# Performance work log

Hardware: AMD Instinct MI355X
Metric: run time of the kernel (lower is better)

The kernel has to match this reference:

```python
import jax, jax.numpy as jnp
import numpy as np

D = 128
N_NODES = 50000
N_EDGES = 500000


def layer_norm(x, g, b, eps=1e-5):
    m = jnp.mean(x, axis=-1, keepdims=True)
    v = jnp.var(x, axis=-1, keepdims=True)
    return (x - m) * jax.lax.rsqrt(v + eps) * g + b


def setup_inputs() -> dict:
    key = jax.random.key(0)
    ks = jax.random.split(key, 10)
    s = 1.0 / np.sqrt(D)  # torch Linear default-ish init scale
    return {
        "src": jax.random.normal(ks[0], (N_NODES, D), jnp.float32),
        "tgt": jax.random.normal(ks[1], (N_NODES, D), jnp.float32),
        "edge": jax.random.normal(ks[2], (N_EDGES, D), jnp.float32),
        "src_idx": jax.random.randint(ks[3], (N_EDGES,), 0, N_NODES, jnp.int64 if jax.config.jax_enable_x64 else jnp.int32),
        "tgt_idx": jax.random.randint(ks[4], (N_EDGES,), 0, N_NODES, jnp.int64 if jax.config.jax_enable_x64 else jnp.int32),
        "W_s2e": jax.random.normal(ks[5], (D, D), jnp.float32) * s,
        "W_t2e": jax.random.normal(ks[6], (D, D), jnp.float32) * s,
        "W_e2e": jax.random.normal(ks[7], (D, D), jnp.float32) * s,
        "W_e2t": jax.random.normal(ks[8], (D, D), jnp.float32) * s,
        "W_t2t": jax.random.normal(ks[9], (D, D), jnp.float32) * s,
        "ln1_g": jnp.ones((D,), jnp.float32),
        "ln1_b": jnp.zeros((D,), jnp.float32),
        "ln2_g": jnp.ones((D,), jnp.float32),
        "ln2_b": jnp.zeros((D,), jnp.float32),
    }


def reference(src, tgt, edge, src_idx, tgt_idx,
              W_s2e, W_t2e, W_e2e, W_e2t, W_t2t,
              ln1_g, ln1_b, ln2_g, ln2_b):
    # ---- STE2E: source/target/edge -> edge update ----
    # gather endpoint node features per edge [E, D]
    msg = (src[src_idx] @ W_s2e.T
           + tgt[tgt_idx] @ W_t2e.T
           + edge @ W_e2e.T)
    edge_out = edge + layer_norm(jax.nn.silu(msg), ln1_g, ln1_b)

    # ---- ET2T: aggregate edges to target nodes, update targets ----
    agg = jax.ops.segment_sum(edge_out, tgt_idx, num_segments=tgt.shape[0])  # [N, D]
    tgt_msg = agg @ W_e2t.T + tgt @ W_t2t.T
    tgt_out = tgt + layer_norm(jax.nn.silu(tgt_msg), ln2_g, ln2_b)

    return edge_out, tgt_out
```

## Files before the change

### kernel.cpp

```cpp
#include <hip/hip_runtime.h>
#include <hip/hip_bf16.h>

#define D 128
#define LDSPAD 136

typedef short s8v __attribute__((ext_vector_type(8)));
typedef float f4v __attribute__((ext_vector_type(4)));

__device__ inline short f2bf(float f) {
    __hip_bfloat16 h = __float2bfloat16(f);
    return *reinterpret_cast<short*>(&h);
}

__device__ inline void load_w_lds(const float* __restrict__ W, short* lds) {
    const int tid = threadIdx.x;
    const float4* W4 = reinterpret_cast<const float4*>(W);
#pragma unroll
    for (int i = 0; i < 16; ++i) {
        int f = tid + 256 * i;
        float4 v = W4[f];
        int row = f >> 5;
        int c4  = (f & 31) * 4;
        short* p = &lds[row * LDSPAD + c4];
        p[0] = f2bf(v.x); p[1] = f2bf(v.y);
        p[2] = f2bf(v.z); p[3] = f2bf(v.w);
    }
}

__device__ inline void mfma_tile(const float* __restrict__ X, int row0,
                                 const short* lds, f4v acc[8]) {
    const int lane = threadIdx.x & 63;
    const int l15 = lane & 15, q = lane >> 4;
    s8v a[4];
    const float* xr = X + (size_t)(row0 + l15) * D + q * 8;
#pragma unroll
    for (int c = 0; c < 4; ++c) {
        float4 f0 = *reinterpret_cast<const float4*>(xr + c * 32);
        float4 f1 = *reinterpret_cast<const float4*>(xr + c * 32 + 4);
        s8v t;
        t[0] = f2bf(f0.x); t[1] = f2bf(f0.y); t[2] = f2bf(f0.z); t[3] = f2bf(f0.w);
        t[4] = f2bf(f1.x); t[5] = f2bf(f1.y); t[6] = f2bf(f1.z); t[7] = f2bf(f1.w);
        a[c] = t;
    }
#pragma unroll
    for (int t = 0; t < 8; ++t) {
        f4v acc_t = {0.f, 0.f, 0.f, 0.f};
#pragma unroll
        for (int c = 0; c < 4; ++c) {
            const s8v b = *reinterpret_cast<const s8v*>(
                &lds[(t * 16 + l15) * LDSPAD + c * 32 + q * 8]);
            acc_t = __builtin_amdgcn_mfma_f32_16x16x32_bf16(a[c], b, acc_t, 0, 0, 0);
        }
        acc[t] = acc_t;
    }
}


__global__ __launch_bounds__(256) void k_zero_i(int* p, int n) {
    int i = blockIdx.x * 256 + threadIdx.x;
    if (i < n) p[i] = 0;
}

__global__ __launch_bounds__(256) void k_hist(const int* __restrict__ tidx,
                                              int* __restrict__ cnt, int E) {
    int i = blockIdx.x * 256 + threadIdx.x;
    if (i < E) atomicAdd(&cnt[tidx[i]], 1);
}

__global__ __launch_bounds__(1024) void k_scan(const int* __restrict__ cnt,
                                               int* __restrict__ off,
                                               int* __restrict__ cursor, int n) {
    __shared__ int part[1024];
    const int tid = threadIdx.x;
    const int chunk = (n + 1023) / 1024;
    const int lo = tid * chunk;
    const int hi = min(lo + chunk, n);
    int s = 0;
    for (int i = lo; i < hi; ++i) s += cnt[i];
    part[tid] = s;
    __syncthreads();
    for (int d = 1; d < 1024; d <<= 1) {
        int v = (tid >= d) ? part[tid - d] : 0;
        __syncthreads();
        part[tid] += v;
        __syncthreads();
    }
    int run = part[tid] - s;
    for (int i = lo; i < hi; ++i) {
        off[i] = run;
        cursor[i] = run;
        run += cnt[i];
    }
    if (tid == 0) off[n] = part[1023];
}

__global__ __launch_bounds__(256) void k_scatter(const int* __restrict__ tidx,
                                                 int* __restrict__ cursor,
                                                 int* __restrict__ elist, int E) {
    int i = blockIdx.x * 256 + threadIdx.x;
    if (i < E) {
        int p = atomicAdd(&cursor[tidx[i]], 1);
        elist[p] = i;
    }
}


__global__ __launch_bounds__(256) void k_node_gemm(const float* __restrict__ X,
                                                   const float* __restrict__ W,
                                                   float* __restrict__ P, int nrows) {
    __shared__ short lds[D * LDSPAD];
    load_w_lds(W, lds);
    __syncthreads();
    const int lane = threadIdx.x & 63, wave = threadIdx.x >> 6;
    const int l15 = lane & 15, q = lane >> 4;
    const int ntiles = nrows >> 4;
    for (int tile = blockIdx.x * 4 + wave; tile < ntiles; tile += gridDim.x * 4) {
        f4v acc[8];
        mfma_tile(X, tile * 16, lds, acc);
#pragma unroll
        for (int t = 0; t < 8; ++t) {
            int col = t * 16 + l15;
#pragma unroll
            for (int r = 0; r < 4; ++r)
                P[(size_t)(tile * 16 + q * 4 + r) * D + col] = acc[t][r];
        }
    }
}

__global__ __launch_bounds__(256) void k_edge(const float* __restrict__ edge,
                                              const int* __restrict__ sidx,
                                              const int* __restrict__ tidx,
                                              const float* __restrict__ W,
                                              const float* __restrict__ Ps,
                                              const float* __restrict__ Pt,
                                              const float* __restrict__ g1,
                                              const float* __restrict__ b1,
                                              float* __restrict__ eout, int E) {
    __shared__ short lds[D * LDSPAD];
    load_w_lds(W, lds);
    __syncthreads();
    const int lane = threadIdx.x & 63, wave = threadIdx.x >> 6;
    const int l15 = lane & 15, q = lane >> 4;
    const int ntiles = E >> 4;
    for (int tile = blockIdx.x * 4 + wave; tile < ntiles; tile += gridDim.x * 4) {
        const int e0 = tile * 16;
        f4v acc[8];
        mfma_tile(edge, e0, lds, acc);
        int si[4], ti[4];
#pragma unroll
        for (int r = 0; r < 4; ++r) {
            si[r] = sidx[e0 + q * 4 + r];
            ti[r] = tidx[e0 + q * 4 + r];
        }
        float h[8][4];
        float s1[4] = {0.f, 0.f, 0.f, 0.f}, s2[4] = {0.f, 0.f, 0.f, 0.f};
#pragma unroll
        for (int t = 0; t < 8; ++t) {
            int col = t * 16 + l15;
#pragma unroll
            for (int r = 0; r < 4; ++r) {
                float m = acc[t][r] + Ps[(size_t)si[r] * D + col]
                                    + Pt[(size_t)ti[r] * D + col];
                float hh = m / (1.f + __expf(-m));
                h[t][r] = hh;
                s1[r] += hh;
                s2[r] += hh * hh;
            }
        }
#pragma unroll
        for (int m = 1; m < 16; m <<= 1) {
#pragma unroll
            for (int r = 0; r < 4; ++r) {
                s1[r] += __shfl_xor(s1[r], m, 64);
                s2[r] += __shfl_xor(s2[r], m, 64);
            }
        }
        float mean[4], rstd[4];
#pragma unroll
        for (int r = 0; r < 4; ++r) {
            float mu = s1[r] * (1.f / 128.f);
            float var = s2[r] * (1.f / 128.f) - mu * mu;
            mean[r] = mu;
            rstd[r] = rsqrtf(var + 1e-5f);
        }
#pragma unroll
        for (int t = 0; t < 8; ++t) {
            int col = t * 16 + l15;
            float gg = g1[col], bb = b1[col];
#pragma unroll
            for (int r = 0; r < 4; ++r) {
                int rowg = e0 + q * 4 + r;
                float v = edge[(size_t)rowg * D + col]
                          + ((h[t][r] - mean[r]) * rstd[r] * gg + bb);
                eout[(size_t)rowg * D + col] = v;
            }
        }
    }
}

__global__ __launch_bounds__(256) void k_agg(const float* __restrict__ eout,
                                             const int* __restrict__ off,
                                             const int* __restrict__ elist,
                                             float* __restrict__ agg, int N) {
    const int node = blockIdx.x * 4 + (threadIdx.x >> 6);
    const int lane = threadIdx.x & 63;
    if (node >= N) return;
    const int lo = off[node], hi = off[node + 1];
    float ax = 0.f, ay = 0.f;
    for (int j = lo; j < hi; ++j) {
        int e = elist[j];
        float2 v = *reinterpret_cast<const float2*>(&eout[(size_t)e * D + 2 * lane]);
        ax += v.x; ay += v.y;
    }
    float2 o = {ax, ay};
    *reinterpret_cast<float2*>(&agg[(size_t)node * D + 2 * lane]) = o;
}

__global__ __launch_bounds__(256) void k_node_update(const float* __restrict__ aggIn,
                                                     const float* __restrict__ W,
                                                     const float* __restrict__ Ptt,
                                                     const float* __restrict__ tgt,
                                                     const float* __restrict__ g2,
                                                     const float* __restrict__ b2,
                                                     float* __restrict__ out, int N) {
    __shared__ short lds[D * LDSPAD];
    load_w_lds(W, lds);
    __syncthreads();
    const int lane = threadIdx.x & 63, wave = threadIdx.x >> 6;
    const int l15 = lane & 15, q = lane >> 4;
    const int ntiles = N >> 4;
    for (int tile = blockIdx.x * 4 + wave; tile < ntiles; tile += gridDim.x * 4) {
        const int n0 = tile * 16;
        f4v acc[8];
        mfma_tile(aggIn, n0, lds, acc);
        float h[8][4];
        float s1[4] = {0.f, 0.f, 0.f, 0.f}, s2[4] = {0.f, 0.f, 0.f, 0.f};
#pragma unroll
        for (int t = 0; t < 8; ++t) {
            int col = t * 16 + l15;
#pragma unroll
            for (int r = 0; r < 4; ++r) {
                int rowg = n0 + q * 4 + r;
                float m = acc[t][r] + Ptt[(size_t)rowg * D + col];
                float hh = m / (1.f + __expf(-m));
                h[t][r] = hh;
                s1[r] += hh;
                s2[r] += hh * hh;
            }
        }
#pragma unroll
        for (int m = 1; m < 16; m <<= 1) {
#pragma unroll
            for (int r = 0; r < 4; ++r) {
                s1[r] += __shfl_xor(s1[r], m, 64);
                s2[r] += __shfl_xor(s2[r], m, 64);
            }
        }
        float mean[4], rstd[4];
#pragma unroll
        for (int r = 0; r < 4; ++r) {
            float mu = s1[r] * (1.f / 128.f);
            float var = s2[r] * (1.f / 128.f) - mu * mu;
            mean[r] = mu;
            rstd[r] = rsqrtf(var + 1e-5f);
        }
#pragma unroll
        for (int t = 0; t < 8; ++t) {
            int col = t * 16 + l15;
            float gg = g2[col], bb = b2[col];
#pragma unroll
            for (int r = 0; r < 4; ++r) {
                int rowg = n0 + q * 4 + r;
                float v = tgt[(size_t)rowg * D + col]
                          + ((h[t][r] - mean[r]) * rstd[r] * gg + bb);
                out[(size_t)rowg * D + col] = v;
            }
        }
    }
}

extern "C" void kernel_launch(void* const* d_in, const int* in_sizes, int n_in,
                              void* d_out, int out_size, void* d_ws, size_t ws_size,
                              hipStream_t stream) {
    const float* src   = (const float*)d_in[0];
    const float* tgt   = (const float*)d_in[1];
    const float* edge  = (const float*)d_in[2];
    const int*   sidx  = (const int*)d_in[3];
    const int*   tidx  = (const int*)d_in[4];
    const float* W_s2e = (const float*)d_in[5];
    const float* W_t2e = (const float*)d_in[6];
    const float* W_e2e = (const float*)d_in[7];
    const float* W_e2t = (const float*)d_in[8];
    const float* W_t2t = (const float*)d_in[9];
    const float* g1    = (const float*)d_in[10];
    const float* b1    = (const float*)d_in[11];
    const float* g2    = (const float*)d_in[12];
    const float* b2    = (const float*)d_in[13];

    const int N = in_sizes[0] / D;
    const int E = in_sizes[3];

    float* eout = (float*)d_out;
    float* nout = eout + (size_t)E * D;

    float* Ps  = (float*)d_ws;
    float* Pt  = Ps + (size_t)N * D;
    float* Ptt = Pt + (size_t)N * D;
    int*   cnt    = (int*)(Ptt + (size_t)N * D);
    int*   off    = cnt + N;
    int*   cursor = off + N + 1;
    int*   elist  = cursor + N;

    k_zero_i<<<(N + 255) / 256, 256, 0, stream>>>(cnt, N);
    k_hist<<<(E + 255) / 256, 256, 0, stream>>>(tidx, cnt, E);
    k_scan<<<1, 1024, 0, stream>>>(cnt, off, cursor, N);
    k_scatter<<<(E + 255) / 256, 256, 0, stream>>>(tidx, cursor, elist, E);

    const int nodeBlocks = (N / 16 + 3) / 4;
    k_node_gemm<<<nodeBlocks, 256, 0, stream>>>(src, W_s2e, Ps, N);
    k_node_gemm<<<nodeBlocks, 256, 0, stream>>>(tgt, W_t2e, Pt, N);
    k_node_gemm<<<nodeBlocks, 256, 0, stream>>>(tgt, W_t2t, Ptt, N);

    k_edge<<<1024, 256, 0, stream>>>(edge, sidx, tidx, W_e2e, Ps, Pt, g1, b1,
                                     eout, E);

    k_agg<<<(N + 3) / 4, 256, 0, stream>>>(eout, off, elist, nout, N);
    k_node_update<<<nodeBlocks, 256, 0, stream>>>(nout, W_e2t, Ptt, tgt, g2, b2,
                                                  nout, N);
}
```

Baseline: 914.5 us.

## Fuse segment-sum into edge kernel via float atomics, drop CSR build

Removes the histogram/scan/scatter CSR construction and the separate gather-based aggregation kernel. Each edge output element is instead atomically added into the node aggregate inside the edge kernel, with the aggregate zeroed by a memset first. It also hoists the LayerNorm gamma/beta loads out of the tile loop and uses a hardware reciprocal in SiLU. The trade is heavy global float atomic traffic (E*D adds) in place of the gather reads, and the summation order becomes nondeterministic.

```diff
diff --git a/kernel.cpp b/kernel.cpp
--- a/kernel.cpp
+++ b/kernel.cpp
@@ -10,6 +10,10 @@
 __device__ inline short f2bf(float f) {
     __hip_bfloat16 h = __float2bfloat16(f);
     return *reinterpret_cast<short*>(&h);
+}
+
+__device__ inline float fast_silu(float m) {
+    return m * __builtin_amdgcn_rcpf(1.f + __expf(-m));
 }
 
 __device__ inline void load_w_lds(const float* __restrict__ W, short* lds) {
@@ -56,55 +60,6 @@
 }
 
 
-__global__ __launch_bounds__(256) void k_zero_i(int* p, int n) {
-    int i = blockIdx.x * 256 + threadIdx.x;
-    if (i < n) p[i] = 0;
-}
-
-__global__ __launch_bounds__(256) void k_hist(const int* __restrict__ tidx,
-                                              int* __restrict__ cnt, int E) {
-    int i = blockIdx.x * 256 + threadIdx.x;
-    if (i < E) atomicAdd(&cnt[tidx[i]], 1);
-}
-
-__global__ __launch_bounds__(1024) void k_scan(const int* __restrict__ cnt,
-                                               int* __restrict__ off,
-                                               int* __restrict__ cursor, int n) {
-    __shared__ int part[1024];
-    const int tid = threadIdx.x;
-    const int chunk = (n + 1023) / 1024;
-    const int lo = tid * chunk;
-    const int hi = min(lo + chunk, n);
-    int s = 0;
-    for (int i = lo; i < hi; ++i) s += cnt[i];
-    part[tid] = s;
-    __syncthreads();
-    for (int d = 1; d < 1024; d <<= 1) {
-        int v = (tid >= d) ? part[tid - d] : 0;
-        __syncthreads();
-        part[tid] += v;
-        __syncthreads();
-    }
-    int run = part[tid] - s;
-    for (int i = lo; i < hi; ++i) {
-        off[i] = run;
-        cursor[i] = run;
-        run += cnt[i];
-    }
-    if (tid == 0) off[n] = part[1023];
-}
-
-__global__ __launch_bounds__(256) void k_scatter(const int* __restrict__ tidx,
-                                                 int* __restrict__ cursor,
-                                                 int* __restrict__ elist, int E) {
-    int i = blockIdx.x * 256 + threadIdx.x;
-    if (i < E) {
-        int p = atomicAdd(&cursor[tidx[i]], 1);
-        elist[p] = i;
-    }
-}
-
-
 __global__ __launch_bounds__(256) void k_node_gemm(const float* __restrict__ X,
                                                    const float* __restrict__ W,
                                                    float* __restrict__ P, int nrows) {
@@ -127,31 +82,38 @@
     }
 }
 
-__global__ __launch_bounds__(256) void k_edge(const float* __restrict__ edge,
-                                              const int* __restrict__ sidx,
-                                              const int* __restrict__ tidx,
-                                              const float* __restrict__ W,
-                                              const float* __restrict__ Ps,
-                                              const float* __restrict__ Pt,
-                                              const float* __restrict__ g1,
-                                              const float* __restrict__ b1,
-                                              float* __restrict__ eout, int E) {
+__global__ __launch_bounds__(256) void k_edge_fused(const float* __restrict__ edge,
+                                                    const int* __restrict__ sidx,
+                                                    const int* __restrict__ tidx,
+                                                    const float* __restrict__ W,
+                                                    const float* __restrict__ Ps,
+                                                    const float* __restrict__ Pt,
+                                                    const float* __restrict__ g1,
+                                                    const float* __restrict__ b1,
+                                                    float* __restrict__ eout,
+                                                    float* __restrict__ agg, int E) {
     __shared__ short lds[D * LDSPAD];
     load_w_lds(W, lds);
     __syncthreads();
     const int lane = threadIdx.x & 63, wave = threadIdx.x >> 6;
     const int l15 = lane & 15, q = lane >> 4;
+    float gg[8], bb[8];
+#pragma unroll
+    for (int t = 0; t < 8; ++t) {
+        gg[t] = g1[t * 16 + l15];
+        bb[t] = b1[t * 16 + l15];
+    }
     const int ntiles = E >> 4;
     for (int tile = blockIdx.x * 4 + wave; tile < ntiles; tile += gridDim.x * 4) {
         const int e0 = tile * 16;
-        f4v acc[8];
-        mfma_tile(edge, e0, lds, acc);
         int si[4], ti[4];
 #pragma unroll
         for (int r = 0; r < 4; ++r) {
             si[r] = sidx[e0 + q * 4 + r];
             ti[r] = tidx[e0 + q * 4 + r];
         }
+        f4v acc[8];
+        mfma_tile(edge, e0, lds, acc);
         float h[8][4];
         float s1[4] = {0.f, 0.f, 0.f, 0.f}, s2[4] = {0.f, 0.f, 0.f, 0.f};
 #pragma unroll
@@ -161,7 +123,7 @@
             for (int r = 0; r < 4; ++r) {
                 float m = acc[t][r] + Ps[(size_t)si[r] * D + col]
                                     + Pt[(size_t)ti[r] * D + col];
-                float hh = m / (1.f + __expf(-m));
+                float hh = fast_silu(m);
                 h[t][r] = hh;
                 s1[r] += hh;
                 s2[r] += hh * hh;
@@ -186,34 +148,16 @@
 #pragma unroll
         for (int t = 0; t < 8; ++t) {
             int col = t * 16 + l15;
-            float gg = g1[col], bb = b1[col];
 #pragma unroll
             for (int r = 0; r < 4; ++r) {
                 int rowg = e0 + q * 4 + r;
                 float v = edge[(size_t)rowg * D + col]
-                          + ((h[t][r] - mean[r]) * rstd[r] * gg + bb);
+                          + ((h[t][r] - mean[r]) * rstd[r] * gg[t] + bb[t]);
                 eout[(size_t)rowg * D + col] = v;
-            }
-        }
-    }
-}
-
-__global__ __launch_bounds__(256) void k_agg(const float* __restrict__ eout,
-                                             const int* __restrict__ off,
-                                             const int* __restrict__ elist,
-                                             float* __restrict__ agg, int N) {
-    const int node = blockIdx.x * 4 + (threadIdx.x >> 6);
-    const int lane = threadIdx.x & 63;
-    if (node >= N) return;
-    const int lo = off[node], hi = off[node + 1];
-    float ax = 0.f, ay = 0.f;
-    for (int j = lo; j < hi; ++j) {
-        int e = elist[j];
-        float2 v = *reinterpret_cast<const float2*>(&eout[(size_t)e * D + 2 * lane]);
-        ax += v.x; ay += v.y;
-    }
-    float2 o = {ax, ay};
-    *reinterpret_cast<float2*>(&agg[(size_t)node * D + 2 * lane]) = o;
+                unsafeAtomicAdd(&agg[(size_t)ti[r] * D + col], v);
+            }
+        }
+    }
 }
 
 __global__ __launch_bounds__(256) void k_node_update(const float* __restrict__ aggIn,
@@ -228,6 +172,12 @@
     __syncthreads();
     const int lane = threadIdx.x & 63, wave = threadIdx.x >> 6;
     const int l15 = lane & 15, q = lane >> 4;
+    float gg[8], bb[8];
+#pragma unroll
+    for (int t = 0; t < 8; ++t) {
+        gg[t] = g2[t * 16 + l15];
+        bb[t] = b2[t * 16 + l15];
+    }
     const int ntiles = N >> 4;
     for (int tile = blockIdx.x * 4 + wave; tile < ntiles; tile += gridDim.x * 4) {
         const int n0 = tile * 16;
@@ -242,7 +192,7 @@
             for (int r = 0; r < 4; ++r) {
                 int rowg = n0 + q * 4 + r;
                 float m = acc[t][r] + Ptt[(size_t)rowg * D + col];
-                float hh = m / (1.f + __expf(-m));
+                float hh = fast_silu(m);
                 h[t][r] = hh;
                 s1[r] += hh;
                 s2[r] += hh * hh;
@@ -267,12 +217,11 @@
 #pragma unroll
         for (int t = 0; t < 8; ++t) {
             int col = t * 16 + l15;
-            float gg = g2[col], bb = b2[col];
 #pragma unroll
             for (int r = 0; r < 4; ++r) {
                 int rowg = n0 + q * 4 + r;
                 float v = tgt[(size_t)rowg * D + col]
-                          + ((h[t][r] - mean[r]) * rstd[r] * gg + bb);
+                          + ((h[t][r] - mean[r]) * rstd[r] * gg[t] + bb[t]);
                 out[(size_t)rowg * D + col] = v;
             }
         }
@@ -306,25 +255,17 @@
     float* Ps  = (float*)d_ws;
     float* Pt  = Ps + (size_t)N * D;
     float* Ptt = Pt + (size_t)N * D;
-    int*   cnt    = (int*)(Ptt + (size_t)N * D);
-    int*   off    = cnt + N;
-    int*   cursor = off + N + 1;
-    int*   elist  = cursor + N;
-
-    k_zero_i<<<(N + 255) / 256, 256, 0, stream>>>(cnt, N);
-    k_hist<<<(E + 255) / 256, 256, 0, stream>>>(tidx, cnt, E);
-    k_scan<<<1, 1024, 0, stream>>>(cnt, off, cursor, N);
-    k_scatter<<<(E + 255) / 256, 256, 0, stream>>>(tidx, cursor, elist, E);
+
+    hipMemsetAsync(nout, 0, (size_t)N * D * sizeof(float), stream);
 
     const int nodeBlocks = (N / 16 + 3) / 4;
     k_node_gemm<<<nodeBlocks, 256, 0, stream>>>(src, W_s2e, Ps, N);
     k_node_gemm<<<nodeBlocks, 256, 0, stream>>>(tgt, W_t2e, Pt, N);
     k_node_gemm<<<nodeBlocks, 256, 0, stream>>>(tgt, W_t2t, Ptt, N);
 
-    k_edge<<<1024, 256, 0, stream>>>(edge, sidx, tidx, W_e2e, Ps, Pt, g1, b1,
-                                     eout, E);
-
-    k_agg<<<(N + 3) / 4, 256, 0, stream>>>(eout, off, elist, nout, N);
+    k_edge_fused<<<1024, 256, 0, stream>>>(edge, sidx, tidx, W_e2e, Ps, Pt,
+                                           g1, b1, eout, nout, E);
+
     k_node_update<<<nodeBlocks, 256, 0, stream>>>(nout, W_e2t, Ptt, tgt, g2, b2,
                                                   nout, N);
 }
```

Result: slower. 985.8 us (+7.8%).
